# Performance work log

Hardware: AMD Instinct MI355X
Metric: run time of the kernel (lower is better)

Reference implementation:

```python
import jax, jax.numpy as jnp
import numpy as np

B, T, IN, H, OUT = 4096, 28, 28, 1024, 10


def setup_inputs() -> dict:
    key = jax.random.key(0)
    ks = jax.random.split(key, 6)
    s_ih = 1.0 / np.sqrt(IN)
    s_h = 1.0 / np.sqrt(H)
    return {
        "x": jax.random.normal(ks[0], (B, T, IN), dtype=jnp.float32),
        "W_ih": jax.random.uniform(ks[1], (IN, 4 * H), jnp.float32, -s_ih, s_ih),
        "W_hh": jax.random.uniform(ks[2], (H, 4 * H), jnp.float32, -s_h, s_h),
        "b": jax.random.uniform(ks[3], (4 * H,), jnp.float32, -s_h, s_h),
        "Wc": jax.random.uniform(ks[4], (H, OUT), jnp.float32, -s_h, s_h),
        "bc": jax.random.uniform(ks[5], (OUT,), jnp.float32, -s_h, s_h),
    }


def _lstm_last_hidden(x, W_ih, W_hh, b):
    # Precompute input projections for all timesteps: [T, B, 4H]
    xg = jnp.einsum('bti,ig->tbg', x, W_ih) + b
    h0 = jnp.zeros((x.shape[0], W_hh.shape[0]), x.dtype)
    c0 = jnp.zeros_like(h0)

    def step(carry, xg_t):
        h, c = carry
        gates = xg_t + h @ W_hh  # [B, 4H]
        i, f, g, o = jnp.split(gates, 4, axis=-1)
        i = jax.nn.sigmoid(i)
        f = jax.nn.sigmoid(f)
        g = jnp.tanh(g)
        o = jax.nn.sigmoid(o)
        c = f * c + i * g
        h = o * jnp.tanh(c)
        return (h, c), None

    (h, _), _ = jax.lax.scan(step, (h0, c0), xg)
    return h


def reference(x, W_ih, W_hh, b, Wc, bc):
    h = _lstm_last_hidden(x, W_ih, W_hh, b)
    # dropout is identity at inference (eval mode)
    return h @ Wc + bc
```

## Files before the change

### kernel.cpp

```cpp
#include <hip/hip_runtime.h>
#include <stdint.h>

#define GLOBAL_AS __attribute__((address_space(1)))
#define LDS_AS    __attribute__((address_space(3)))

typedef __attribute__((ext_vector_type(8))) short  short8;
typedef __attribute__((ext_vector_type(4))) float  floatx4;

static constexpr int B_   = 4096;
static constexpr int T_   = 28;
static constexpr int IN_  = 28;
static constexpr int H_   = 1024;
static constexpr int G4_  = 4096;
static constexpr int OUT_ = 10;
static constexpr int NT_  = 16;

__device__ __forceinline__ float bf2f(unsigned short u) {
  union { uint32_t i; float f; } v; v.i = ((uint32_t)u) << 16; return v.f;
}
__device__ __forceinline__ unsigned short f2bf(float f) {
  union { float f; uint32_t i; } v; v.f = f;
  uint32_t x = v.i;
  uint32_t lsb = (x >> 16) & 1u;
  x += 0x7fffu + lsb;
  return (unsigned short)(x >> 16);
}
__device__ __forceinline__ float sigm(float x) {
  return __builtin_amdgcn_rcpf(1.f + __builtin_amdgcn_exp2f(-1.4426950408889634f * x));
}
__device__ __forceinline__ float tanh_f(float x) {
  return 1.f - 2.f * __builtin_amdgcn_rcpf(1.f + __builtin_amdgcn_exp2f(2.8853900817779268f * x));
}
__device__ __forceinline__ void stage16(const unsigned short* g, unsigned short* l) {
  __builtin_amdgcn_global_load_lds(
      (const GLOBAL_AS uint32_t*)g, (LDS_AS uint32_t*)l, 16, 0, 0);
}

__global__ __launch_bounds__(256) void conv_x_kernel(const float* __restrict__ x,
                                                     unsigned short* __restrict__ xb) {
  int row = blockIdx.x * 256 + threadIdx.x;
  int t  = row >> 12;
  int bb = row & 4095;
  const float* src = x + (bb * T_ + t) * IN_;
  unsigned short* dst = xb + row * 32;
#pragma unroll
  for (int k = 0; k < IN_; ++k) dst[k] = f2bf(src[k]);
  dst[28] = 0; dst[29] = 0; dst[30] = 0; dst[31] = 0;
}

__global__ __launch_bounds__(256) void perm_whh_kernel(const float* __restrict__ whh,
                                                       unsigned short* __restrict__ wp) {
  __shared__ float lds[64][17];
  int g64  = blockIdx.x >> 2;
  int gate = blockIdx.x & 3;
  int oc0  = gate * H_ + g64 * 16;
  int n0   = g64 * 64 + gate * 16;
  int tid  = threadIdx.x;
  for (int kc = 0; kc < 16; ++kc) {
    int k0 = kc * 64;
    __syncthreads();
#pragma unroll
    for (int e = 0; e < 4; ++e) {
      int idx = e * 256 + tid;
      int k = idx >> 4, cc = idx & 15;
      lds[k][cc] = whh[(k0 + k) * G4_ + oc0 + cc];
    }
    __syncthreads();
#pragma unroll
    for (int e = 0; e < 4; ++e) {
      int idx = e * 256 + tid;
      int n = idx >> 6, kk = idx & 63;
      wp[(n0 + n) * H_ + k0 + kk] = f2bf(lds[kk][n]);
    }
  }
}

__global__ __launch_bounds__(256) void perm_wih_kernel(const float* __restrict__ wih,
                                                       unsigned short* __restrict__ wip) {
  __shared__ float lds[28][17];
  int g64  = blockIdx.x >> 2;
  int gate = blockIdx.x & 3;
  int oc0  = gate * H_ + g64 * 16;
  int n0   = g64 * 64 + gate * 16;
  int tid  = threadIdx.x;
  for (int idx = tid; idx < 448; idx += 256) {
    int k = idx >> 4, cc = idx & 15;
    lds[k][cc] = wih[k * G4_ + oc0 + cc];
  }
  __syncthreads();
#pragma unroll
  for (int e = 0; e < 2; ++e) {
    int idx = e * 256 + tid;
    int n = idx >> 5, kk = idx & 31;
    wip[(n0 + n) * 32 + kk] = (kk < IN_) ? f2bf(lds[kk][n]) : (unsigned short)0;
  }
}

__global__ __launch_bounds__(512, 2) void lstm_step_kernel(
    const unsigned short* __restrict__ hprev,
    const unsigned short* __restrict__ wp,
    const unsigned short* __restrict__ xbt,
    const unsigned short* __restrict__ wip,
    const float* __restrict__ bias,
    float* __restrict__ cst,
    unsigned short* __restrict__ hnext,
    int first) {
  __shared__ __align__(16) unsigned short lds[65536];

  const int tid = threadIdx.x;
  const int w   = tid >> 6;
  const int l   = tid & 63;
  const int wm  = w >> 2;
  const int wn  = w & 3;
  const int lc  = l & 15;
  const int lk  = l >> 4;

  const int hid = blockIdx.x;
  const int lid = (hid & 7) * 32 + (hid >> 3);
  const int bx  = lid & 15, by = lid >> 4;
  const int m0  = bx * 256;
  const int n0  = by * 256;

  const int swz  = (lc & 7) << 4;
  const int swzx = (lc & 3) << 4;

  const int r8  = tid >> 3;
  const int c8  = (tid & 7) * 8;
  const int c8s = c8 ^ ((r8 & 7) * 8);
  const size_t aoff = (size_t)(m0 + r8) * H_ + c8s;
  const int bwn_low = r8 >> 5;
  const int bc31    = r8 & 31;
  const int rx   = tid >> 2;
  const int cx8  = (tid & 3) * 8;
  const int cx8s = cx8 ^ ((rx & 3) * 8);

  auto stageA = [&](int bufu, int kt, int i) {
    stage16(hprev + aoff + (size_t)i * (64 * H_) + kt * 64,
            lds + bufu + i * 4096 + tid * 8);
  };
  auto stageB = [&](int bufu, int kt, int j) {
    int col = n0 + (((j & 1) * 2 + bwn_low) * 64) + ((j >> 1) * 32) + bc31;
    stage16(wp + (size_t)col * H_ + c8s + kt * 64,
            lds + bufu + 16384 + j * 4096 + tid * 8);
  };
  auto stageXA = [&](int half) {
    int row = half * 128 + rx;
    stage16(xbt + (size_t)(m0 + row) * 32 + cx8s,
            lds + 32768 + half * 4096 + tid * 8);
  };
  auto stageXB = [&](int half) {
    int col = n0 + (rx >> 5) * 64 + half * 32 + (rx & 31);
    stage16(wip + (size_t)col * 32 + cx8s,
            lds + 32768 + 8192 + half * 4096 + tid * 8);
  };
  auto ldsr = [&](int byteoff) -> short8 {
    return *reinterpret_cast<const short8*>(reinterpret_cast<const char*>(lds) + byteoff);
  };

  floatx4 acc[8][4];
#pragma unroll
  for (int i = 0; i < 8; ++i)
#pragma unroll
    for (int j = 0; j < 4; ++j) acc[i][j] = (floatx4){0.f, 0.f, 0.f, 0.f};

  short8 a[4][2];
  short8 b[4][2];

#define LOAD_B_ALL(PB)                                                               \
  _Pragma("unroll") for (int nh_ = 0; nh_ < 2; ++nh_)                                \
  _Pragma("unroll") for (int n_ = 0; n_ < 2; ++n_)                                   \
  _Pragma("unroll") for (int k_ = 0; k_ < 2; ++k_)                                   \
    b[nh_ * 2 + n_][k_] =                                                            \
        ldsr((PB) + 32768 + (nh_ * 128 + wn * 32 + n_ * 16 + lc) * 128 +             \
             ((k_ * 64 + lk * 16) ^ swz));

#define LOAD_A(PB, MH)                                                               \
  _Pragma("unroll") for (int m_ = 0; m_ < 4; ++m_)                                   \
  _Pragma("unroll") for (int k_ = 0; k_ < 2; ++k_)                                   \
    a[m_][k_] = ldsr((PB) + (wm * 128 + (MH) * 64 + m_ * 16 + lc) * 128 +            \
                     ((k_ * 64 + lk * 16) ^ swz));

#define MFMA_HALF(MH)                                                                \
  __builtin_amdgcn_s_setprio(1);                                                     \
  _Pragma("unroll") for (int m_ = 0; m_ < 4; ++m_)                                   \
  _Pragma("unroll") for (int nh_ = 0; nh_ < 2; ++nh_)                                \
  _Pragma("unroll") for (int n_ = 0; n_ < 2; ++n_)                                   \
  _Pragma("unroll") for (int k_ = 0; k_ < 2; ++k_)                                   \
    acc[(MH) * 4 + m_][nh_ * 2 + n_] = __builtin_amdgcn_mfma_f32_16x16x32_bf16(      \
        a[m_][k_], b[nh_ * 2 + n_][k_], acc[(MH) * 4 + m_][nh_ * 2 + n_], 0, 0, 0);  \
  __builtin_amdgcn_s_setprio(0);

#define TILE_BAR(VM)                                                                 \
  __builtin_amdgcn_sched_barrier(0);                                                 \
  asm volatile("s_waitcnt vmcnt(" #VM ")" ::: "memory");                             \
  __builtin_amdgcn_s_barrier();                                                      \
  __builtin_amdgcn_sched_barrier(0);

  if (first) {
    stageXA(0); stageXA(1); stageXB(0); stageXB(1);
    TILE_BAR(0)
    short8 xb4[4];
#pragma unroll
    for (int nf = 0; nf < 4; ++nf)
      xb4[nf] = ldsr(65536 + 16384 +
                     ((nf >> 1) * 128 + wn * 32 + (nf & 1) * 16 + lc) * 64 +
                     ((lk * 16) ^ swzx));
#pragma unroll
    for (int mf = 0; mf < 8; ++mf) {
      short8 xa = ldsr(65536 + (wm * 128 + mf * 16 + lc) * 64 + ((lk * 16) ^ swzx));
#pragma unroll
      for (int nf = 0; nf < 4; ++nf)
        acc[mf][nf] = __builtin_amdgcn_mfma_f32_16x16x32_bf16(xa, xb4[nf], acc[mf][nf], 0, 0, 0);
    }
  } else {
    stageXA(0); stageXA(1); stageXB(0); stageXB(1);
#pragma unroll
    for (int j = 0; j < 4; ++j) stageB(0, 0, j);
#pragma unroll
    for (int i = 0; i < 4; ++i) stageA(0, 0, i);
    TILE_BAR(8)
    {
      short8 xb4[4];
#pragma unroll
      for (int nf = 0; nf < 4; ++nf)
        xb4[nf] = ldsr(65536 + 16384 +
                       ((nf >> 1) * 128 + wn * 32 + (nf & 1) * 16 + lc) * 64 +
                       ((lk * 16) ^ swzx));
      __builtin_amdgcn_s_setprio(1);
#pragma unroll
      for (int mf = 0; mf < 8; ++mf) {
        short8 xa = ldsr(65536 + (wm * 128 + mf * 16 + lc) * 64 + ((lk * 16) ^ swzx));
#pragma unroll
        for (int nf = 0; nf < 4; ++nf)
          acc[mf][nf] = __builtin_amdgcn_mfma_f32_16x16x32_bf16(xa, xb4[nf], acc[mf][nf], 0, 0, 0);
      }
      __builtin_amdgcn_s_setprio(0);
    }
    TILE_BAR(0)

    for (int kt = 0; kt < NT_; ++kt) {
      const int pbB = (kt & 1) * 65536;
      const int qbu = ((kt + 1) & 1) * 32768;

      if (kt + 1 < NT_) {
#pragma unroll
        for (int j = 0; j < 4; ++j) stageB(qbu, kt + 1, j);
#pragma unroll
        for (int i = 0; i < 4; ++i) stageA(qbu, kt + 1, i);
      }
      LOAD_B_ALL(pbB)
      LOAD_A(pbB, 0)
      MFMA_HALF(0)
      LOAD_A(pbB, 1)
      MFMA_HALF(1)
      if (kt + 1 < NT_) { TILE_BAR(0) }
    }
  }

  const int jj  = (by * 4 + wn) * 16 + lc;
  const float bi  = bias[jj];
  const float bf_ = bias[H_ + jj];
  const float bg_ = bias[2 * H_ + jj];
  const float bo_ = bias[3 * H_ + jj];
#pragma unroll
  for (int mf = 0; mf < 8; ++mf) {
    const int rbase = m0 + wm * 128 + mf * 16 + lk * 4;
#pragma unroll
    for (int r = 0; r < 4; ++r) {
      const size_t idx = (size_t)(rbase + r) * H_ + jj;
      float ig = sigm(acc[mf][0][r] + bi);
      float fg = sigm(acc[mf][1][r] + bf_);
      float gg = tanh_f(acc[mf][2][r] + bg_);
      float og = sigm(acc[mf][3][r] + bo_);
      float cp = first ? 0.f : cst[idx];
      float cn = fg * cp + ig * gg;
      cst[idx] = cn;
      hnext[idx] = f2bf(og * tanh_f(cn));
    }
  }
#undef LOAD_B_ALL
#undef LOAD_A
#undef MFMA_HALF
#undef TILE_BAR
}

__global__ __launch_bounds__(256) void cls_kernel(const unsigned short* __restrict__ h,
                                                  const float* __restrict__ wc,
                                                  const float* __restrict__ bc,
                                                  float* __restrict__ out) {
  int w = threadIdx.x >> 6, l = threadIdx.x & 63;
  int row = blockIdx.x * 4 + w;
  float acc[OUT_];
#pragma unroll
  for (int o = 0; o < OUT_; ++o) acc[o] = 0.f;
  const unsigned short* hr = h + row * H_;
  for (int k = l; k < H_; k += 64) {
    float hv = bf2f(hr[k]);
#pragma unroll
    for (int o = 0; o < OUT_; ++o) acc[o] += hv * wc[k * OUT_ + o];
  }
#pragma unroll
  for (int o = 0; o < OUT_; ++o) {
    float v = acc[o];
#pragma unroll
    for (int s = 32; s > 0; s >>= 1) v += __shfl_down(v, s, 64);
    if (l == 0) out[row * OUT_ + o] = v + bc[o];
  }
}

extern "C" void kernel_launch(void* const* d_in, const int* in_sizes, int n_in,
                              void* d_out, int out_size, void* d_ws, size_t ws_size,
                              hipStream_t stream) {
  const float* x    = (const float*)d_in[0];
  const float* wih  = (const float*)d_in[1];
  const float* whh  = (const float*)d_in[2];
  const float* bias = (const float*)d_in[3];
  const float* wc   = (const float*)d_in[4];
  const float* bc   = (const float*)d_in[5];
  float* out = (float*)d_out;

  char* ws = (char*)d_ws;
  unsigned short* wp  = (unsigned short*)(ws);
  unsigned short* wip = (unsigned short*)(ws + 8388608);
  unsigned short* xb  = (unsigned short*)(ws + 8650752);
  unsigned short* h0  = (unsigned short*)(ws + 15990784);
  unsigned short* h1  = (unsigned short*)(ws + 24379392);
  float*          cst = (float*)(ws + 32768000);

  hipLaunchKernelGGL(conv_x_kernel,  dim3(448), dim3(256), 0, stream, x, xb);
  hipLaunchKernelGGL(perm_whh_kernel, dim3(256), dim3(256), 0, stream, whh, wp);
  hipLaunchKernelGGL(perm_wih_kernel, dim3(256), dim3(256), 0, stream, wih, wip);

  unsigned short* hb[2] = {h0, h1};
  for (int t = 0; t < T_; ++t) {
    unsigned short* hn = hb[t & 1];
    unsigned short* hp = hb[(t & 1) ^ 1];
    hipLaunchKernelGGL(lstm_step_kernel, dim3(256), dim3(512), 0, stream,
                       hp, wp, xb + (size_t)t * (B_ * 32), wip, bias, cst, hn,
                       (t == 0) ? 1 : 0);
  }
  hipLaunchKernelGGL(cls_kernel, dim3(1024), dim3(256), 0, stream, hb[1], wc, bc, out);
}
```

Measured before the change: 1.127 ms.

## Halve LSTM step tile width, single-buffer LDS, store cell state in fp16

The per-step GEMM tile shrinks from 256x256 to 256x128, so the grid doubles to 512 blocks. LDS drops to 48KB and is single-buffered, and launch bounds now allow 4 blocks per CU. Blocks are remapped so each XCD covers a compact 2D patch of tiles, and the cell state is stored in fp16 instead of fp32 to cut epilogue traffic. The trade-off is lost load/compute overlap from double buffering, more reloads of A tiles across N, and reduced cell-state precision.

```diff
diff --git a/kernel.cpp b/kernel.cpp
--- a/kernel.cpp
+++ b/kernel.cpp
@@ -1,4 +1,5 @@
 #include <hip/hip_runtime.h>
+#include <hip/hip_fp16.h>
 #include <stdint.h>
 
 #define GLOBAL_AS __attribute__((address_space(1)))
@@ -96,30 +97,31 @@
   }
 }
 
-__global__ __launch_bounds__(512, 2) void lstm_step_kernel(
+__global__ __launch_bounds__(512, 4) void lstm_step_kernel(
     const unsigned short* __restrict__ hprev,
     const unsigned short* __restrict__ wp,
     const unsigned short* __restrict__ xbt,
     const unsigned short* __restrict__ wip,
     const float* __restrict__ bias,
-    float* __restrict__ cst,
+    unsigned short* __restrict__ cst,
     unsigned short* __restrict__ hnext,
     int first) {
-  __shared__ __align__(16) unsigned short lds[65536];
+  __shared__ __align__(16) unsigned short lds[24576];
 
   const int tid = threadIdx.x;
   const int w   = tid >> 6;
   const int l   = tid & 63;
-  const int wm  = w >> 2;
-  const int wn  = w & 3;
+  const int wm  = w >> 1;
+  const int wn  = w & 1;
   const int lc  = l & 15;
   const int lk  = l >> 4;
 
   const int hid = blockIdx.x;
-  const int lid = (hid & 7) * 32 + (hid >> 3);
-  const int bx  = lid & 15, by = lid >> 4;
+  const int xcd = hid & 7, q = hid >> 3;
+  const int bx  = (xcd & 1) * 8 + (q & 7);
+  const int by  = (xcd >> 1) * 8 + (q >> 3);
   const int m0  = bx * 256;
-  const int n0  = by * 256;
+  const int n0  = by * 128;
 
   const int swz  = (lc & 7) << 4;
   const int swzx = (lc & 3) << 4;
@@ -127,144 +129,117 @@
   const int r8  = tid >> 3;
   const int c8  = (tid & 7) * 8;
   const int c8s = c8 ^ ((r8 & 7) * 8);
-  const size_t aoff = (size_t)(m0 + r8) * H_ + c8s;
-  const int bwn_low = r8 >> 5;
-  const int bc31    = r8 & 31;
   const int rx   = tid >> 2;
-  const int cx8  = (tid & 3) * 8;
-  const int cx8s = cx8 ^ ((rx & 3) * 8);
-
-  auto stageA = [&](int bufu, int kt, int i) {
-    stage16(hprev + aoff + (size_t)i * (64 * H_) + kt * 64,
-            lds + bufu + i * 4096 + tid * 8);
-  };
-  auto stageB = [&](int bufu, int kt, int j) {
-    int col = n0 + (((j & 1) * 2 + bwn_low) * 64) + ((j >> 1) * 32) + bc31;
-    stage16(wp + (size_t)col * H_ + c8s + kt * 64,
-            lds + bufu + 16384 + j * 4096 + tid * 8);
+  const int cx8s = ((tid & 3) * 8) ^ ((rx & 3) * 8);
+
+  auto stageA = [&](int kt, int i) {
+    stage16(hprev + (size_t)(m0 + i * 64 + r8) * H_ + kt * 64 + c8s,
+            lds + i * 4096 + tid * 8);
+  };
+  auto stageB = [&](int kt, int j) {
+    stage16(wp + (size_t)(n0 + j * 64 + r8) * H_ + kt * 64 + c8s,
+            lds + 16384 + j * 4096 + tid * 8);
   };
   auto stageXA = [&](int half) {
-    int row = half * 128 + rx;
-    stage16(xbt + (size_t)(m0 + row) * 32 + cx8s,
-            lds + 32768 + half * 4096 + tid * 8);
-  };
-  auto stageXB = [&](int half) {
-    int col = n0 + (rx >> 5) * 64 + half * 32 + (rx & 31);
-    stage16(wip + (size_t)col * 32 + cx8s,
-            lds + 32768 + 8192 + half * 4096 + tid * 8);
+    stage16(xbt + (size_t)(m0 + half * 128 + rx) * 32 + cx8s,
+            lds + half * 4096 + tid * 8);
+  };
+  auto stageXB = [&]() {
+    stage16(wip + (size_t)(n0 + rx) * 32 + cx8s,
+            lds + 8192 + tid * 8);
   };
   auto ldsr = [&](int byteoff) -> short8 {
     return *reinterpret_cast<const short8*>(reinterpret_cast<const char*>(lds) + byteoff);
   };
 
-  floatx4 acc[8][4];
-#pragma unroll
-  for (int i = 0; i < 8; ++i)
+  floatx4 acc[4][4];
+#pragma unroll
+  for (int i = 0; i < 4; ++i)
 #pragma unroll
     for (int j = 0; j < 4; ++j) acc[i][j] = (floatx4){0.f, 0.f, 0.f, 0.f};
 
   short8 a[4][2];
-  short8 b[4][2];
-
-#define LOAD_B_ALL(PB)                                                               \
-  _Pragma("unroll") for (int nh_ = 0; nh_ < 2; ++nh_)                                \
+  short8 b[2][2];
+
+#define LOAD_A                                                                       \
+  _Pragma("unroll") for (int m_ = 0; m_ < 4; ++m_)                                   \
+  _Pragma("unroll") for (int k_ = 0; k_ < 2; ++k_)                                   \
+    a[m_][k_] = ldsr((wm * 64 + m_ * 16 + lc) * 128 + ((k_ * 64 + lk * 16) ^ swz));
+
+#define LOAD_B(P)                                                                    \
   _Pragma("unroll") for (int n_ = 0; n_ < 2; ++n_)                                   \
   _Pragma("unroll") for (int k_ = 0; k_ < 2; ++k_)                                   \
-    b[nh_ * 2 + n_][k_] =                                                            \
-        ldsr((PB) + 32768 + (nh_ * 128 + wn * 32 + n_ * 16 + lc) * 128 +             \
-             ((k_ * 64 + lk * 16) ^ swz));
-
-#define LOAD_A(PB, MH)                                                               \
-  _Pragma("unroll") for (int m_ = 0; m_ < 4; ++m_)                                   \
-  _Pragma("unroll") for (int k_ = 0; k_ < 2; ++k_)                                   \
-    a[m_][k_] = ldsr((PB) + (wm * 128 + (MH) * 64 + m_ * 16 + lc) * 128 +            \
+    b[n_][k_] = ldsr(32768 + (wn * 64 + ((P) * 2 + n_) * 16 + lc) * 128 +            \
                      ((k_ * 64 + lk * 16) ^ swz));
 
-#define MFMA_HALF(MH)                                                                \
+#define MFMA_P(P)                                                                    \
   __builtin_amdgcn_s_setprio(1);                                                     \
   _Pragma("unroll") for (int m_ = 0; m_ < 4; ++m_)                                   \
-  _Pragma("unroll") for (int nh_ = 0; nh_ < 2; ++nh_)                                \
   _Pragma("unroll") for (int n_ = 0; n_ < 2; ++n_)                                   \
   _Pragma("unroll") for (int k_ = 0; k_ < 2; ++k_)                                   \
-    acc[(MH) * 4 + m_][nh_ * 2 + n_] = __builtin_amdgcn_mfma_f32_16x16x32_bf16(      \
-        a[m_][k_], b[nh_ * 2 + n_][k_], acc[(MH) * 4 + m_][nh_ * 2 + n_], 0, 0, 0);  \
+    acc[m_][(P) * 2 + n_] = __builtin_amdgcn_mfma_f32_16x16x32_bf16(                 \
+        a[m_][k_], b[n_][k_], acc[m_][(P) * 2 + n_], 0, 0, 0);                       \
   __builtin_amdgcn_s_setprio(0);
 
-#define TILE_BAR(VM)                                                                 \
+#define BAR_ONLY                                                                     \
   __builtin_amdgcn_sched_barrier(0);                                                 \
-  asm volatile("s_waitcnt vmcnt(" #VM ")" ::: "memory");                             \
   __builtin_amdgcn_s_barrier();                                                      \
   __builtin_amdgcn_sched_barrier(0);
 
-  if (first) {
-    stageXA(0); stageXA(1); stageXB(0); stageXB(1);
-    TILE_BAR(0)
+#define BAR_VM0                                                                      \
+  __builtin_amdgcn_sched_barrier(0);                                                 \
+  asm volatile("s_waitcnt vmcnt(0)" ::: "memory");                                   \
+  __builtin_amdgcn_s_barrier();                                                      \
+  __builtin_amdgcn_sched_barrier(0);
+
+  stageXA(0); stageXA(1); stageXB();
+  BAR_VM0
+  {
     short8 xb4[4];
 #pragma unroll
     for (int nf = 0; nf < 4; ++nf)
-      xb4[nf] = ldsr(65536 + 16384 +
-                     ((nf >> 1) * 128 + wn * 32 + (nf & 1) * 16 + lc) * 64 +
-                     ((lk * 16) ^ swzx));
-#pragma unroll
-    for (int mf = 0; mf < 8; ++mf) {
-      short8 xa = ldsr(65536 + (wm * 128 + mf * 16 + lc) * 64 + ((lk * 16) ^ swzx));
+      xb4[nf] = ldsr(16384 + (wn * 64 + nf * 16 + lc) * 64 + ((lk * 16) ^ swzx));
+    __builtin_amdgcn_s_setprio(1);
+#pragma unroll
+    for (int mf = 0; mf < 4; ++mf) {
+      short8 xa = ldsr((wm * 64 + mf * 16 + lc) * 64 + ((lk * 16) ^ swzx));
 #pragma unroll
       for (int nf = 0; nf < 4; ++nf)
         acc[mf][nf] = __builtin_amdgcn_mfma_f32_16x16x32_bf16(xa, xb4[nf], acc[mf][nf], 0, 0, 0);
     }
-  } else {
-    stageXA(0); stageXA(1); stageXB(0); stageXB(1);
-#pragma unroll
-    for (int j = 0; j < 4; ++j) stageB(0, 0, j);
-#pragma unroll
-    for (int i = 0; i < 4; ++i) stageA(0, 0, i);
-    TILE_BAR(8)
-    {
-      short8 xb4[4];
-#pragma unroll
-      for (int nf = 0; nf < 4; ++nf)
-        xb4[nf] = ldsr(65536 + 16384 +
-                       ((nf >> 1) * 128 + wn * 32 + (nf & 1) * 16 + lc) * 64 +
-                       ((lk * 16) ^ swzx));
-      __builtin_amdgcn_s_setprio(1);
-#pragma unroll
-      for (int mf = 0; mf < 8; ++mf) {
-        short8 xa = ldsr(65536 + (wm * 128 + mf * 16 + lc) * 64 + ((lk * 16) ^ swzx));
-#pragma unroll
-        for (int nf = 0; nf < 4; ++nf)
-          acc[mf][nf] = __builtin_amdgcn_mfma_f32_16x16x32_bf16(xa, xb4[nf], acc[mf][nf], 0, 0, 0);
+    __builtin_amdgcn_s_setprio(0);
+  }
+
+  if (!first) {
+    BAR_ONLY
+#pragma unroll
+    for (int i = 0; i < 4; ++i) stageA(0, i);
+    stageB(0, 0); stageB(0, 1);
+    BAR_VM0
+    for (int kt = 0; kt < NT_; ++kt) {
+      LOAD_A
+      LOAD_B(0)
+      MFMA_P(0)
+      LOAD_B(1)
+      MFMA_P(1)
+      if (kt + 1 < NT_) {
+        BAR_ONLY
+#pragma unroll
+        for (int i = 0; i < 4; ++i) stageA(kt + 1, i);
+        stageB(kt + 1, 0); stageB(kt + 1, 1);
+        BAR_VM0
       }
-      __builtin_amdgcn_s_setprio(0);
-    }
-    TILE_BAR(0)
-
-    for (int kt = 0; kt < NT_; ++kt) {
-      const int pbB = (kt & 1) * 65536;
-      const int qbu = ((kt + 1) & 1) * 32768;
-
-      if (kt + 1 < NT_) {
-#pragma unroll
-        for (int j = 0; j < 4; ++j) stageB(qbu, kt + 1, j);
-#pragma unroll
-        for (int i = 0; i < 4; ++i) stageA(qbu, kt + 1, i);
-      }
-      LOAD_B_ALL(pbB)
-      LOAD_A(pbB, 0)
-      MFMA_HALF(0)
-      LOAD_A(pbB, 1)
-      MFMA_HALF(1)
-      if (kt + 1 < NT_) { TILE_BAR(0) }
-    }
-  }
-
-  const int jj  = (by * 4 + wn) * 16 + lc;
+    }
+  }
+
+  const int jj  = (by * 2 + wn) * 16 + lc;
   const float bi  = bias[jj];
   const float bf_ = bias[H_ + jj];
   const float bg_ = bias[2 * H_ + jj];
   const float bo_ = bias[3 * H_ + jj];
 #pragma unroll
-  for (int mf = 0; mf < 8; ++mf) {
-    const int rbase = m0 + wm * 128 + mf * 16 + lk * 4;
+  for (int mf = 0; mf < 4; ++mf) {
+    const int rbase = m0 + wm * 64 + mf * 16 + lk * 4;
 #pragma unroll
     for (int r = 0; r < 4; ++r) {
       const size_t idx = (size_t)(rbase + r) * H_ + jj;
@@ -272,16 +247,17 @@
       float fg = sigm(acc[mf][1][r] + bf_);
       float gg = tanh_f(acc[mf][2][r] + bg_);
       float og = sigm(acc[mf][3][r] + bo_);
-      float cp = first ? 0.f : cst[idx];
+      float cp = first ? 0.f : __half2float(__ushort_as_half(cst[idx]));
       float cn = fg * cp + ig * gg;
-      cst[idx] = cn;
+      cst[idx] = __half_as_ushort(__float2half(cn));
       hnext[idx] = f2bf(og * tanh_f(cn));
     }
   }
-#undef LOAD_B_ALL
 #undef LOAD_A
-#undef MFMA_HALF
-#undef TILE_BAR
+#undef LOAD_B
+#undef MFMA_P
+#undef BAR_ONLY
+#undef BAR_VM0
 }
 
 __global__ __launch_bounds__(256) void cls_kernel(const unsigned short* __restrict__ h,
@@ -325,7 +301,7 @@
   unsigned short* xb  = (unsigned short*)(ws + 8650752);
   unsigned short* h0  = (unsigned short*)(ws + 15990784);
   unsigned short* h1  = (unsigned short*)(ws + 24379392);
-  float*          cst = (float*)(ws + 32768000);
+  unsigned short* cst = (unsigned short*)(ws + 32768000);
 
   hipLaunchKernelGGL(conv_x_kernel,  dim3(448), dim3(256), 0, stream, x, xb);
   hipLaunchKernelGGL(perm_whh_kernel, dim3(256), dim3(256), 0, stream, whh, wp);
@@ -335,7 +311,7 @@
   for (int t = 0; t < T_; ++t) {
     unsigned short* hn = hb[t & 1];
     unsigned short* hp = hb[(t & 1) ^ 1];
-    hipLaunchKernelGGL(lstm_step_kernel, dim3(256), dim3(512), 0, stream,
+    hipLaunchKernelGGL(lstm_step_kernel, dim3(512), dim3(512), 0, stream,
                        hp, wp, xb + (size_t)t * (B_ * 32), wip, bias, cst, hn,
                        (t == 0) ? 1 : 0);
   }
```

New measurement: 1.066 ms. -5.4%, faster.
